# Kernel tuning notes

Measured on AMD Instinct MI355X. Metric: run time of the kernel, lower is better.

## Reference

```python
import jax, jax.numpy as jnp
import numpy as np

H, G, D = 16, 4, 64  # heads, n_global, head_dim
DM = H * D           # 1024 hidden size
B, N = 8, 4096


def setup_inputs() -> dict:
    key = jax.random.key(0)
    ks = jax.random.split(key, 16)
    std = 0.02
    def lin(k, fi, fo):
        return jax.random.normal(k, (fi, fo), dtype=jnp.float32) * std
    return {
        "hidden_states": jax.random.normal(ks[0], (B, N, DM), dtype=jnp.float32),
        "attention_mask": jnp.zeros((B, 1, N), dtype=jnp.float32),
        "Wq": lin(ks[1], DM, DM), "bq": jnp.zeros((DM,), jnp.float32),
        "Wqa": lin(ks[2], DM, H * G), "bqa": jnp.zeros((H * G,), jnp.float32),
        "Wk": lin(ks[3], DM, DM), "bk": jnp.zeros((DM,), jnp.float32),
        "Wka": lin(ks[4], DM, H * G), "bka": jnp.zeros((H * G,), jnp.float32),
        "Wv": lin(ks[5], DM, DM), "bv": jnp.zeros((DM,), jnp.float32),
        "Wt": lin(ks[6], DM, DM), "bt": jnp.zeros((DM,), jnp.float32),
    }


def reference(hidden_states, attention_mask, Wq, bq, Wqa, bqa, Wk, bk, Wka, bka, Wv, bv, Wt, bt):
    b, n, _ = hidden_states.shape
    scale = D ** 0.5
    q = hidden_states @ Wq + bq            # b n (h d)
    k = hidden_states @ Wk + bk
    v = hidden_states @ Wv + bv
    # query attention scores: b n (h g) -> b h g n
    qs = (q @ Wqa + bqa).reshape(b, n, H, G).transpose(0, 2, 3, 1) / scale
    qs = qs + attention_mask[:, None]      # broadcast over h (and g)
    qw = jax.nn.softmax(qs, axis=-1)       # b h g n
    mq = q.reshape(b, n, H, D).transpose(0, 2, 1, 3)   # b h n d
    gq = jnp.einsum('bhgn,bhnd->bhdg', qw, mq)          # b h d g
    kh = k.reshape(b, n, H, D).transpose(0, 2, 1, 3)    # b h n d
    qk = kh[..., None] * gq[:, :, None]                 # b h n d g
    qk = qk.transpose(0, 2, 1, 3, 4).reshape(b, n, H * D, G)
    qk = jnp.max(qk, axis=-1)                           # b n (h d)
    # NOTE: original code adds mask but does NOT softmax this score
    ksc = (qk @ Wka + bka).reshape(b, n, H, G).transpose(0, 2, 3, 1) / scale
    ksc = ksc + attention_mask[:, None]                 # b h g n
    gk = jnp.einsum('bhgn,bhnd->bhdg', ksc, kh)         # b h d g
    vh = v.reshape(b, n, H, D).transpose(0, 2, 1, 3)    # b h n d
    u = gk[:, :, None] * vh[..., None]                  # b h n d g
    u = jnp.max(u, axis=-1)                             # b h n d
    u = u.transpose(0, 2, 1, 3).reshape(b, n, H * D)    # b n (h d)
    r = u @ Wt + bt
    return r + q
```

## Files before the change

kernel.cpp:

```cpp
#include <hip/hip_runtime.h>
#include <hip/hip_bf16.h>

typedef __bf16 bf16;
typedef __attribute__((ext_vector_type(8))) __bf16 bf16x8;
typedef __attribute__((ext_vector_type(4))) float floatx4;


__device__ __forceinline__ void gload_lds16(const void* g, void* l) {
    __builtin_amdgcn_global_load_lds(
        (const __attribute__((address_space(1))) unsigned int*)g,
        (__attribute__((address_space(3))) unsigned int*)l, 16, 0, 0);
}

#define WAIT_VM(N) asm volatile("s_waitcnt vmcnt(" #N ")" ::: "memory")

__global__ __launch_bounds__(256)
void cvt_kernel(const float* __restrict__ src, bf16* __restrict__ dst, int n8) {
    int i8 = blockIdx.x * 256 + threadIdx.x;
    if (i8 >= n8) return;
    const float* s = src + (size_t)i8 * 8;
    float4 x = *(const float4*)s;
    float4 y = *(const float4*)(s + 4);
    bf16x8 o;
    o[0] = (bf16)x.x; o[1] = (bf16)x.y; o[2] = (bf16)x.z; o[3] = (bf16)x.w;
    o[4] = (bf16)y.x; o[5] = (bf16)y.y; o[6] = (bf16)y.z; o[7] = (bf16)y.w;
    *(bf16x8*)(dst + (size_t)i8 * 8) = o;
}

__global__ __launch_bounds__(256)
void transpose_cvt_kernel(const float* __restrict__ src, bf16* __restrict__ dst, int R, int C) {
    __shared__ bf16 tile[64][65];
    int tr0 = blockIdx.x * 64;
    int tc0 = blockIdx.y * 64;
    int tx = threadIdx.x & 63, ty = threadIdx.x >> 6;
#pragma unroll
    for (int j = 0; j < 16; j++) {
        int r = ty + j * 4;
        tile[tx][r] = (bf16)src[(size_t)(tr0 + r) * C + tc0 + tx];
    }
    __syncthreads();
#pragma unroll
    for (int j = 0; j < 16; j++) {
        int r = ty + j * 4;
        dst[(size_t)(tc0 + r) * R + tr0 + tx] = tile[r][tx];
    }
}

__global__ __launch_bounds__(256)
void biaspack_kernel(const float* __restrict__ bq, const float* __restrict__ bk,
                     const float* __restrict__ bv, float* __restrict__ biasf,
                     float* __restrict__ zbias) {
    int i = blockIdx.x * 256 + threadIdx.x;
    if (i < 1024)      biasf[i] = bq[i];
    else if (i < 2048) biasf[i] = bk[i - 1024];
    else if (i < 3072) biasf[i] = bv[i - 2048];
    else if (i < 3200) biasf[i] = 0.f;
    else if (i < 4224) zbias[i - 3200] = 0.f;
}

__global__ __launch_bounds__(64)
void compbias_kernel(const float* __restrict__ bq, const float* __restrict__ Wqa,
                     const float* __restrict__ bqa, float* __restrict__ out) {
    int j = threadIdx.x;
    float a = 0.f;
    for (int t = 0; t < 1024; t++) a += bq[t] * Wqa[(size_t)t * 64 + j];
    out[j] = a + bqa[j];
}

template<int BN, int WN, int EPI>
__global__ __launch_bounds__(WN * 128)
void gemm_kernel(const bf16* __restrict__ A, int lda,
                 const bf16* __restrict__ WT,
                 const float* __restrict__ bias,
                 void* __restrict__ Cout, int ldc,
                 const float* __restrict__ mask,
                 const bf16* __restrict__ qadd, int ldq,
                 int K) {
    constexpr int BM = 128;
    constexpr int NT = WN * 128;
    __shared__ bf16 As[BM * 32];
    __shared__ bf16 Bs[BN * 32];

    const int tid  = threadIdx.x;
    const int wid  = tid >> 6;
    const int lane = tid & 63;
    const int l16  = lane & 15;
    const int quad = lane >> 4;
    const int wm   = wid & 1;
    const int wn   = wid >> 1;
    const int m0   = blockIdx.x * BM;
    const int n0   = blockIdx.y * BN;

    floatx4 acc[4][4];
#pragma unroll
    for (int i = 0; i < 4; i++)
#pragma unroll
        for (int j = 0; j < 4; j++) acc[i][j] = (floatx4)0.0f;

    for (int k0 = 0; k0 < K; k0 += 32) {
        __syncthreads();
#pragma unroll
        for (int i = tid; i < BM * 4; i += NT) {
            const bf16* gp = A + (size_t)(m0 + (i >> 2)) * lda + k0 + (i & 3) * 8;
            gload_lds16(gp, (char*)As + (size_t)(i & ~63) * 16);
        }
#pragma unroll
        for (int i = tid; i < BN * 4; i += NT) {
            const bf16* gp = WT + (size_t)(n0 + (i >> 2)) * K + k0 + (i & 3) * 8;
            gload_lds16(gp, (char*)Bs + (size_t)(i & ~63) * 16);
        }
        __syncthreads();
        bf16x8 af[4], bfv[4];
#pragma unroll
        for (int mi = 0; mi < 4; mi++)
            af[mi] = *(const bf16x8*)&As[(wm * 64 + mi * 16 + l16) * 32 + quad * 8];
#pragma unroll
        for (int ni = 0; ni < 4; ni++)
            bfv[ni] = *(const bf16x8*)&Bs[(wn * 64 + ni * 16 + l16) * 32 + quad * 8];
#pragma unroll
        for (int mi = 0; mi < 4; mi++)
#pragma unroll
            for (int ni = 0; ni < 4; ni++)
                acc[mi][ni] = __builtin_amdgcn_mfma_f32_16x16x32_bf16(
                    af[mi], bfv[ni], acc[mi][ni], 0, 0, 0);
    }

#pragma unroll
    for (int mi = 0; mi < 4; mi++) {
#pragma unroll
        for (int ni = 0; ni < 4; ni++) {
            int col  = n0 + wn * 64 + ni * 16 + l16;
            int rowb = m0 + wm * 64 + mi * 16 + quad * 4;
            float bv = bias[col];
#pragma unroll
            for (int e = 0; e < 4; e++) {
                int row = rowb + e;
                float v = acc[mi][ni][e] + bv;
                if (EPI == 0) {
                    ((bf16*)Cout)[(size_t)row * ldc + col] = (bf16)v;
                } else if (EPI == 2) {
                    ((float*)Cout)[(size_t)row * ldc + col] = v * 0.125f + mask[row];
                } else {
                    v += (float)qadd[(size_t)row * ldq + col];
                    ((float*)Cout)[(size_t)row * ldc + col] = v;
                }
            }
        }
    }
}

#define STG_A(KT) do { \
    gload_lds16(gA0 + (KT) * 32, sA + (((KT) & 3) << 14)); \
    gload_lds16(gA1 + (KT) * 32, sA + (((KT) & 3) << 14) + 1024); } while (0)
#define STG_B(KT) do { \
    gload_lds16(gB0 + (KT) * 32, sB + (((KT) & 3) << 14)); \
    gload_lds16(gB1 + (KT) * 32, sB + (((KT) & 3) << 14) + 1024); } while (0)
#define RD_AFA(T) { _Pragma("unroll") for (int r_ = 0; r_ < 4; ++r_) \
    af_a[r_] = *(const bf16x8*)(lA + (((T) & 3) << 14) + r_ * 1024); }
#define RD_AFB(T) { _Pragma("unroll") for (int r_ = 0; r_ < 4; ++r_) \
    af_b[r_] = *(const bf16x8*)(lA + (((T) & 3) << 14) + 4096 + r_ * 1024); }
#define RD_BFV(T, S) { _Pragma("unroll") for (int n_ = 0; n_ < 4; ++n_) \
    bfv[S][n_] = *(const bf16x8*)(lB + (((T) & 3) << 14) + n_ * 1024); }
#define MM_HALF(MH, S) { _Pragma("unroll") for (int r_ = 0; r_ < 4; ++r_) \
    _Pragma("unroll") for (int n_ = 0; n_ < 4; ++n_) \
    acc[(MH) * 4 + r_][n_] = __builtin_amdgcn_mfma_f32_16x16x32_bf16( \
        (MH) ? af_b[r_] : af_a[r_], bfv[S][n_], acc[(MH) * 4 + r_][n_], 0, 0, 0); }

template<int EPI>
__global__ __launch_bounds__(512, 2)
void gemm256_kernel(const bf16* __restrict__ A, int lda,
                    const bf16* __restrict__ B, int ldb,
                    const float* __restrict__ bias,
                    void* __restrict__ Cout, int ldc, int ncols,
                    const bf16* __restrict__ qadd, int ldq,
                    int ntn) {
    constexpr int NT = 32;
    extern __shared__ __align__(16) char smem[];
    const int tid  = threadIdx.x;
    const int wid  = tid >> 6;
    const int lane = tid & 63;
    const int l16  = lane & 15;
    const int quad = lane >> 4;
    const int wm   = wid >> 2;
    const int wn   = wid & 3;

    const int nwg  = gridDim.x * gridDim.y;
    const int orig = blockIdx.y * gridDim.x + blockIdx.x;
    int swz = orig;
    if ((nwg & 7) == 0) swz = (orig & 7) * (nwg >> 3) + (orig >> 3);
    const int m0 = (swz / ntn) * 256;
    const int n0 = (swz % ntn) * 256;

    const int srow = wid * 32 + (lane >> 2);
    const int scol = ((lane & 3) ^ ((lane >> 5) << 1)) << 3;
    const bf16* gA0 = A + (size_t)(m0 + srow) * lda + scol;
    const bf16* gA1 = gA0 + (size_t)16 * lda;
    const bf16* gB0 = B + (size_t)(n0 + srow) * ldb + scol;
    const bf16* gB1 = gB0 + (size_t)16 * ldb;
    char* sA = smem + wid * 2048;
    char* sB = smem + 65536 + wid * 2048;
    const int aoff = (l16 * 64 + quad * 16) ^ ((l16 & 8) << 2);
    const char* lA = smem + wm * 8192 + aoff;
    const char* lB = smem + 65536 + wn * 4096 + aoff;

    floatx4 acc[8][4];
#pragma unroll
    for (int i = 0; i < 8; ++i)
#pragma unroll
        for (int j = 0; j < 4; ++j) acc[i][j] = (floatx4)0.0f;

    bf16x8 af_a[4], af_b[4], bfv[2][4];

    STG_A(0); STG_B(0); STG_A(1); STG_B(1); STG_A(2); STG_B(2);
    WAIT_VM(8);
    __builtin_amdgcn_s_barrier();
    RD_AFA(0);
    RD_BFV(0, 0);

#pragma unroll
    for (int t = 0; t < NT; ++t) {
        RD_AFB(t);
        if (t + 3 < NT) STG_A(t + 3);
        __builtin_amdgcn_s_barrier();
        __builtin_amdgcn_s_setprio(1);
        MM_HALF(0, t & 1);
        __builtin_amdgcn_s_setprio(0);
        if (t < NT - 3)       { WAIT_VM(6); }
        else if (t == NT - 3) { WAIT_VM(4); }
        else if (t == NT - 2) { WAIT_VM(0); }
        __builtin_amdgcn_s_barrier();

        if (t + 1 < NT) { RD_AFA(t + 1); RD_BFV(t + 1, (t + 1) & 1); }
        if (t + 3 < NT) STG_B(t + 3);
        __builtin_amdgcn_s_barrier();
        __builtin_amdgcn_s_setprio(1);
        MM_HALF(1, t & 1);
        __builtin_amdgcn_s_setprio(0);
        __builtin_amdgcn_s_barrier();
    }

#pragma unroll
    for (int mi = 0; mi < 8; ++mi) {
#pragma unroll
        for (int ni = 0; ni < 4; ++ni) {
            int col  = n0 + wn * 64 + ni * 16 + l16;
            int rowb = m0 + wm * 128 + mi * 16 + quad * 4;
            if (col < ncols) {
                float bv = bias[col];
#pragma unroll
                for (int e = 0; e < 4; ++e) {
                    int row = rowb + e;
                    float v = acc[mi][ni][e] + bv;
                    if (EPI == 0) {
                        ((bf16*)Cout)[(size_t)row * ldc + col] = (bf16)v;
                    } else {
                        v += (float)qadd[(size_t)row * ldq + col];
                        ((float*)Cout)[(size_t)row * ldc + col] = v;
                    }
                }
            }
        }
    }
}

__global__ __launch_bounds__(256)
void softmax_kernel(const bf16* __restrict__ qkv, const float* __restrict__ mask,
                    float* __restrict__ qw) {
    int bh = blockIdx.x;
    int b = bh >> 6, hg = bh & 63;
    int tid = threadIdx.x;
    float xs[16];
    float mx = -1e30f;
#pragma unroll
    for (int j = 0; j < 16; j++) {
        int n = tid + j * 256;
        float x = (float)qkv[(size_t)(b * 4096 + n) * 3200 + 3072 + hg] * 0.125f
                  + mask[b * 4096 + n];
        xs[j] = x;
        mx = fmaxf(mx, x);
    }
    __shared__ float red[256];
    red[tid] = mx;
    __syncthreads();
    for (int s = 128; s > 0; s >>= 1) {
        if (tid < s) red[tid] = fmaxf(red[tid], red[tid + s]);
        __syncthreads();
    }
    mx = red[0];
    __syncthreads();
    float sum = 0.f;
#pragma unroll
    for (int j = 0; j < 16; j++) { xs[j] = __expf(xs[j] - mx); sum += xs[j]; }
    red[tid] = sum;
    __syncthreads();
    for (int s = 128; s > 0; s >>= 1) {
        if (tid < s) red[tid] += red[tid + s];
        __syncthreads();
    }
    float inv = 1.0f / red[0];
#pragma unroll
    for (int j = 0; j < 16; j++)
        qw[(size_t)bh * 4096 + tid + j * 256] = xs[j] * inv;
}

__global__ __launch_bounds__(256)
void gq1_kernel(const float* __restrict__ qw, const bf16* __restrict__ qkv,
                float* __restrict__ part) {
    int bh = blockIdx.x, ch = blockIdx.y;
    int b = bh >> 4, h = bh & 15;
    int tid = threadIdx.x;
    int g = tid >> 6, d = tid & 63;
    const float* wrow = qw + ((size_t)(b * 64 + h * 4 + g)) * 4096 + ch * 256;
    const bf16* qcol  = qkv + (size_t)(b * 4096 + ch * 256) * 3200 + h * 64 + d;
    float a = 0.f;
#pragma unroll 8
    for (int n = 0; n < 256; n++)
        a += wrow[n] * (float)qcol[(size_t)n * 3200];
    part[(((size_t)bh * 16 + ch) * 4 + g) * 64 + d] = a;
}

__global__ __launch_bounds__(256)
void gk1_kernel(const float* __restrict__ ksc, const bf16* __restrict__ qkv,
                float* __restrict__ part) {
    int bh = blockIdx.x, ch = blockIdx.y;
    int b = bh >> 4, h = bh & 15;
    int tid = threadIdx.x;
    int g = tid >> 6, d = tid & 63;
    const float* sbase = ksc + (size_t)(b * 4096 + ch * 256) * 64 + h * 4 + g;
    const bf16* kcol   = qkv + (size_t)(b * 4096 + ch * 256) * 3200 + 1024 + h * 64 + d;
    float a = 0.f;
#pragma unroll 8
    for (int n = 0; n < 256; n++)
        a += sbase[(size_t)n * 64] * (float)kcol[(size_t)n * 3200];
    part[(((size_t)bh * 16 + ch) * 4 + g) * 64 + d] = a;
}

__global__ __launch_bounds__(256)
void gred_kernel(const float* __restrict__ part,
                 float* __restrict__ gmax, float* __restrict__ gmin) {
    int bh = blockIdx.x;
    int tid = threadIdx.x;
    int g = tid >> 6, d = tid & 63;
    float a = 0.f;
#pragma unroll
    for (int c = 0; c < 16; c++)
        a += part[(((size_t)bh * 16 + c) * 4 + g) * 64 + d];
    __shared__ float sg[4][64];
    sg[g][d] = a;
    __syncthreads();
    if (tid < 64) {
        float mx = sg[0][tid], mn = sg[0][tid];
#pragma unroll
        for (int gg = 1; gg < 4; gg++) {
            mx = fmaxf(mx, sg[gg][tid]);
            mn = fminf(mn, sg[gg][tid]);
        }
        gmax[bh * 64 + tid] = mx;
        gmin[bh * 64 + tid] = mn;
    }
}

__global__ __launch_bounds__(256)
void maxg_kernel(const bf16* __restrict__ qkv, int coloff,
                 const float* __restrict__ gmax, const float* __restrict__ gmin,
                 bf16* __restrict__ dst) {
    size_t i8 = (size_t)blockIdx.x * 256 + threadIdx.x;
    size_t e0 = i8 * 8;
    int row = (int)(e0 >> 10);
    int c   = (int)(e0 & 1023);
    int b   = row >> 12;
    bf16x8 kv = *(const bf16x8*)(qkv + (size_t)row * 3200 + coloff + c);
    bf16x8 out;
#pragma unroll
    for (int j = 0; j < 8; j++) {
        float f  = (float)kv[j];
        float gm = gmax[b * 1024 + c + j];
        float gn = gmin[b * 1024 + c + j];
        out[j] = (bf16)(f >= 0.f ? f * gm : f * gn);
    }
    *(bf16x8*)(dst + e0) = out;
}

extern "C" void kernel_launch(void* const* d_in, const int* in_sizes, int n_in,
                              void* d_out, int out_size, void* d_ws, size_t ws_size,
                              hipStream_t stream) {
    const float* hs   = (const float*)d_in[0];
    const float* mask = (const float*)d_in[1];
    const float* Wq   = (const float*)d_in[2];
    const float* bq   = (const float*)d_in[3];
    const float* Wqa  = (const float*)d_in[4];
    const float* bqa  = (const float*)d_in[5];
    const float* Wk   = (const float*)d_in[6];
    const float* bk   = (const float*)d_in[7];
    const float* Wka  = (const float*)d_in[8];
    const float* bka  = (const float*)d_in[9];
    const float* Wv   = (const float*)d_in[10];
    const float* bv   = (const float*)d_in[11];
    const float* Wt   = (const float*)d_in[12];
    const float* bt   = (const float*)d_in[13];

    char* p = (char*)d_ws;
    auto alloc = [&](size_t bytes) {
        char* r = p;
        p += (bytes + 255) & ~(size_t)255;
        return (void*)r;
    };
    bf16*  WT    = (bf16*) alloc((size_t)3328 * 1024 * 2);
    bf16*  WqBf  = (bf16*) alloc((size_t)1024 * 1024 * 2);
    bf16*  WqaT  = (bf16*) alloc((size_t)128 * 1024 * 2);
    bf16*  WkaT  = (bf16*) alloc((size_t)64 * 1024 * 2);
    bf16*  WtT   = (bf16*) alloc((size_t)1024 * 1024 * 2);
    float* biasf = (float*)alloc((size_t)3200 * 4);
    float* zbias = (float*)alloc((size_t)1024 * 4);
    bf16*  qkv   = (bf16*) alloc((size_t)32768 * 3200 * 2);
    bf16*  hsb   = (bf16*) alloc((size_t)32768 * 1024 * 2);
    float* qw    = (float*)alloc((size_t)512 * 4096 * 4);
    float* part  = (float*)alloc((size_t)128 * 16 * 256 * 4);
    float* gqmax = (float*)alloc((size_t)8192 * 4);
    float* gqmin = (float*)alloc((size_t)8192 * 4);
    float* gkmax = (float*)alloc((size_t)8192 * 4);
    float* gkmin = (float*)alloc((size_t)8192 * 4);
    bf16*  qk_u  = hsb;
    float* ksc   = qw;

    (void)hipFuncSetAttribute(reinterpret_cast<const void*>(&gemm256_kernel<0>),
                              hipFuncAttributeMaxDynamicSharedMemorySize, 131072);
    (void)hipFuncSetAttribute(reinterpret_cast<const void*>(&gemm256_kernel<3>),
                              hipFuncAttributeMaxDynamicSharedMemorySize, 131072);

    cvt_kernel<<<16384, 256, 0, stream>>>(hs, hsb, 4194304);
    cvt_kernel<<<512, 256, 0, stream>>>(Wq, WqBf, 131072);
    transpose_cvt_kernel<<<dim3(16, 16), 256, 0, stream>>>(Wq, WT, 1024, 1024);
    transpose_cvt_kernel<<<dim3(16, 16), 256, 0, stream>>>(Wk, WT + (size_t)1024 * 1024, 1024, 1024);
    transpose_cvt_kernel<<<dim3(16, 16), 256, 0, stream>>>(Wv, WT + (size_t)2048 * 1024, 1024, 1024);
    transpose_cvt_kernel<<<dim3(16, 1), 256, 0, stream>>>(Wqa, WqaT, 1024, 64);
    transpose_cvt_kernel<<<dim3(16, 1), 256, 0, stream>>>(Wka, WkaT, 1024, 64);
    transpose_cvt_kernel<<<dim3(16, 16), 256, 0, stream>>>(Wt, WtT, 1024, 1024);
    biaspack_kernel<<<17, 256, 0, stream>>>(bq, bk, bv, biasf, zbias);
    compbias_kernel<<<1, 64, 0, stream>>>(bq, Wqa, bqa, biasf + 3072);
    gemm_kernel<128, 2, 0><<<dim3(1, 8), 256, 0, stream>>>(
        WqaT, 1024, WqBf, zbias, WT + (size_t)3072 * 1024, 1024, nullptr, nullptr, 0, 1024);

    gemm256_kernel<0><<<dim3(128, 13), 512, 131072, stream>>>(
        hsb, 1024, WT, 1024, biasf, qkv, 3200, 3200, nullptr, 0, 13);
    softmax_kernel<<<512, 256, 0, stream>>>(qkv, mask, qw);
    gq1_kernel<<<dim3(128, 16), 256, 0, stream>>>(qw, qkv, part);
    gred_kernel<<<128, 256, 0, stream>>>(part, gqmax, gqmin);
    maxg_kernel<<<16384, 256, 0, stream>>>(qkv, 1024, gqmax, gqmin, qk_u);
    gemm_kernel<64, 1, 2><<<dim3(256, 1), 128, 0, stream>>>(
        qk_u, 1024, WkaT, bka, ksc, 64, mask, nullptr, 0, 1024);
    gk1_kernel<<<dim3(128, 16), 256, 0, stream>>>(ksc, qkv, part);
    gred_kernel<<<128, 256, 0, stream>>>(part, gkmax, gkmin);
    maxg_kernel<<<16384, 256, 0, stream>>>(qkv, 2048, gkmax, gkmin, qk_u);
    gemm256_kernel<3><<<dim3(128, 4), 512, 131072, stream>>>(
        qk_u, 1024, WtT, 1024, bt, d_out, 1024, 1024, qkv, 3200, 4);
}
```

Baseline: 906.6 us.

## Shrink big GEMM tile to 256x128 with 3-stage single-barrier pipeline

The large GEMM kernel now uses a 256x128 output tile per 512-thread block. Each wave owns a 64x64 sub-tile, so it holds half the accumulators. The K loop becomes a 3-slot LDS ring with one barrier and one MFMA batch per step, replacing the 4-slot split-half schedule. LDS drops to 72KB and launch bounds ask for 4 waves per SIMD, so more blocks can be resident and the grids double. The cost is lower arithmetic intensity per block, with more global and LDS traffic per FLOP and less overlap between LDS reads and MFMA inside each block.

```diff
diff --git a/kernel.cpp b/kernel.cpp
--- a/kernel.cpp
+++ b/kernel.cpp
@@ -149,25 +149,25 @@
     }
 }
 
-#define STG_A(KT) do { \
-    gload_lds16(gA0 + (KT) * 32, sA + (((KT) & 3) << 14)); \
-    gload_lds16(gA1 + (KT) * 32, sA + (((KT) & 3) << 14) + 1024); } while (0)
-#define STG_B(KT) do { \
-    gload_lds16(gB0 + (KT) * 32, sB + (((KT) & 3) << 14)); \
-    gload_lds16(gB1 + (KT) * 32, sB + (((KT) & 3) << 14) + 1024); } while (0)
-#define RD_AFA(T) { _Pragma("unroll") for (int r_ = 0; r_ < 4; ++r_) \
-    af_a[r_] = *(const bf16x8*)(lA + (((T) & 3) << 14) + r_ * 1024); }
-#define RD_AFB(T) { _Pragma("unroll") for (int r_ = 0; r_ < 4; ++r_) \
-    af_b[r_] = *(const bf16x8*)(lA + (((T) & 3) << 14) + 4096 + r_ * 1024); }
-#define RD_BFV(T, S) { _Pragma("unroll") for (int n_ = 0; n_ < 4; ++n_) \
-    bfv[S][n_] = *(const bf16x8*)(lB + (((T) & 3) << 14) + n_ * 1024); }
-#define MM_HALF(MH, S) { _Pragma("unroll") for (int r_ = 0; r_ < 4; ++r_) \
-    _Pragma("unroll") for (int n_ = 0; n_ < 4; ++n_) \
-    acc[(MH) * 4 + r_][n_] = __builtin_amdgcn_mfma_f32_16x16x32_bf16( \
-        (MH) ? af_b[r_] : af_a[r_], bfv[S][n_], acc[(MH) * 4 + r_][n_], 0, 0, 0); }
+#define STG(KT) do {                                                       \
+    gload_lds16(gA0 + (KT) * 32, sA + ((KT) % 3) * 24576);                 \
+    gload_lds16(gA1 + (KT) * 32, sA + ((KT) % 3) * 24576 + 1024);          \
+    gload_lds16(gB0 + (KT) * 32, sB + ((KT) % 3) * 24576); } while (0)
+
+#define RDF(SLOT) {                                                        \
+    _Pragma("unroll") for (int i_ = 0; i_ < 4; ++i_)                       \
+        af[i_] = *(const bf16x8*)(lA + (SLOT) * 24576 + i_ * 1024);        \
+    _Pragma("unroll") for (int i_ = 0; i_ < 4; ++i_)                       \
+        bq_[i_] = *(const bf16x8*)(lB + (SLOT) * 24576 + i_ * 1024); }
+
+#define MM() {                                                             \
+    _Pragma("unroll") for (int mi_ = 0; mi_ < 4; ++mi_)                    \
+    _Pragma("unroll") for (int ni_ = 0; ni_ < 4; ++ni_)                    \
+        acc[mi_][ni_] = __builtin_amdgcn_mfma_f32_16x16x32_bf16(           \
+            af[mi_], bq_[ni_], acc[mi_][ni_], 0, 0, 0); }
 
 template<int EPI>
-__global__ __launch_bounds__(512, 2)
+__global__ __launch_bounds__(512, 4)
 void gemm256_kernel(const bf16* __restrict__ A, int lda,
                     const bf16* __restrict__ B, int ldb,
                     const float* __restrict__ bias,
@@ -181,70 +181,55 @@
     const int lane = tid & 63;
     const int l16  = lane & 15;
     const int quad = lane >> 4;
-    const int wm   = wid >> 2;
-    const int wn   = wid & 3;
+    const int wm   = wid >> 1;
+    const int wn   = wid & 1;
 
     const int nwg  = gridDim.x * gridDim.y;
     const int orig = blockIdx.y * gridDim.x + blockIdx.x;
     int swz = orig;
     if ((nwg & 7) == 0) swz = (orig & 7) * (nwg >> 3) + (orig >> 3);
     const int m0 = (swz / ntn) * 256;
-    const int n0 = (swz % ntn) * 256;
-
-    const int srow = wid * 32 + (lane >> 2);
+    const int n0 = (swz % ntn) * 128;
+
     const int scol = ((lane & 3) ^ ((lane >> 5) << 1)) << 3;
-    const bf16* gA0 = A + (size_t)(m0 + srow) * lda + scol;
+    const bf16* gA0 = A + (size_t)(m0 + wid * 32 + (lane >> 2)) * lda + scol;
     const bf16* gA1 = gA0 + (size_t)16 * lda;
-    const bf16* gB0 = B + (size_t)(n0 + srow) * ldb + scol;
-    const bf16* gB1 = gB0 + (size_t)16 * ldb;
+    const bf16* gB0 = B + (size_t)(n0 + wid * 16 + (lane >> 2)) * ldb + scol;
     char* sA = smem + wid * 2048;
-    char* sB = smem + 65536 + wid * 2048;
+    char* sB = smem + 16384 + wid * 1024;
     const int aoff = (l16 * 64 + quad * 16) ^ ((l16 & 8) << 2);
-    const char* lA = smem + wm * 8192 + aoff;
-    const char* lB = smem + 65536 + wn * 4096 + aoff;
-
-    floatx4 acc[8][4];
-#pragma unroll
-    for (int i = 0; i < 8; ++i)
+    const char* lA = smem + wm * 4096 + aoff;
+    const char* lB = smem + 16384 + wn * 4096 + aoff;
+
+    floatx4 acc[4][4];
+#pragma unroll
+    for (int i = 0; i < 4; ++i)
 #pragma unroll
         for (int j = 0; j < 4; ++j) acc[i][j] = (floatx4)0.0f;
 
-    bf16x8 af_a[4], af_b[4], bfv[2][4];
-
-    STG_A(0); STG_B(0); STG_A(1); STG_B(1); STG_A(2); STG_B(2);
-    WAIT_VM(8);
+    STG(0); STG(1);
+    WAIT_VM(3);
     __builtin_amdgcn_s_barrier();
-    RD_AFA(0);
-    RD_BFV(0, 0);
 
 #pragma unroll
     for (int t = 0; t < NT; ++t) {
-        RD_AFB(t);
-        if (t + 3 < NT) STG_A(t + 3);
-        __builtin_amdgcn_s_barrier();
+        if (t + 2 < NT) STG(t + 2);
+        bf16x8 af[4], bq_[4];
+        RDF(t % 3);
         __builtin_amdgcn_s_setprio(1);
-        MM_HALF(0, t & 1);
+        MM();
         __builtin_amdgcn_s_setprio(0);
-        if (t < NT - 3)       { WAIT_VM(6); }
-        else if (t == NT - 3) { WAIT_VM(4); }
+        if (t <= NT - 3)      { WAIT_VM(3); }
         else if (t == NT - 2) { WAIT_VM(0); }
-        __builtin_amdgcn_s_barrier();
-
-        if (t + 1 < NT) { RD_AFA(t + 1); RD_BFV(t + 1, (t + 1) & 1); }
-        if (t + 3 < NT) STG_B(t + 3);
-        __builtin_amdgcn_s_barrier();
-        __builtin_amdgcn_s_setprio(1);
-        MM_HALF(1, t & 1);
-        __builtin_amdgcn_s_setprio(0);
-        __builtin_amdgcn_s_barrier();
-    }
-
-#pragma unroll
-    for (int mi = 0; mi < 8; ++mi) {
+        if (t < NT - 1) __builtin_amdgcn_s_barrier();
+    }
+
+#pragma unroll
+    for (int mi = 0; mi < 4; ++mi) {
 #pragma unroll
         for (int ni = 0; ni < 4; ++ni) {
             int col  = n0 + wn * 64 + ni * 16 + l16;
-            int rowb = m0 + wm * 128 + mi * 16 + quad * 4;
+            int rowb = m0 + wm * 64 + mi * 16 + quad * 4;
             if (col < ncols) {
                 float bv = bias[col];
 #pragma unroll
@@ -424,9 +409,9 @@
     float* ksc   = qw;
 
     (void)hipFuncSetAttribute(reinterpret_cast<const void*>(&gemm256_kernel<0>),
-                              hipFuncAttributeMaxDynamicSharedMemorySize, 131072);
+                              hipFuncAttributeMaxDynamicSharedMemorySize, 73728);
     (void)hipFuncSetAttribute(reinterpret_cast<const void*>(&gemm256_kernel<3>),
-                              hipFuncAttributeMaxDynamicSharedMemorySize, 131072);
+                              hipFuncAttributeMaxDynamicSharedMemorySize, 73728);
 
     cvt_kernel<<<16384, 256, 0, stream>>>(hs, hsb, 4194304);
     cvt_kernel<<<512, 256, 0, stream>>>(Wq, WqBf, 131072);
@@ -441,8 +426,8 @@
     gemm_kernel<128, 2, 0><<<dim3(1, 8), 256, 0, stream>>>(
         WqaT, 1024, WqBf, zbias, WT + (size_t)3072 * 1024, 1024, nullptr, nullptr, 0, 1024);
 
-    gemm256_kernel<0><<<dim3(128, 13), 512, 131072, stream>>>(
-        hsb, 1024, WT, 1024, biasf, qkv, 3200, 3200, nullptr, 0, 13);
+    gemm256_kernel<0><<<dim3(128, 26), 512, 73728, stream>>>(
+        hsb, 1024, WT, 1024, biasf, qkv, 3200, 3200, nullptr, 0, 26);
     softmax_kernel<<<512, 256, 0, stream>>>(qkv, mask, qw);
     gq1_kernel<<<dim3(128, 16), 256, 0, stream>>>(qw, qkv, part);
     gred_kernel<<<128, 256, 0, stream>>>(part, gqmax, gqmin);
@@ -452,6 +437,6 @@
     gk1_kernel<<<dim3(128, 16), 256, 0, stream>>>(ksc, qkv, part);
     gred_kernel<<<128, 256, 0, stream>>>(part, gkmax, gkmin);
     maxg_kernel<<<16384, 256, 0, stream>>>(qkv, 2048, gkmax, gkmin, qk_u);
-    gemm256_kernel<3><<<dim3(128, 4), 512, 131072, stream>>>(
-        qk_u, 1024, WtT, 1024, bt, d_out, 1024, 1024, qkv, 3200, 4);
-}
+    gemm256_kernel<3><<<dim3(128, 8), 512, 73728, stream>>>(
+        qk_u, 1024, WtT, 1024, bt, d_out, 1024, 1024, qkv, 3200, 8);
+}
```

Measured after the change: 916.6 us. Within noise of the previous version (+1.1%).
